# Optimization experiments

Hardware: AMD Instinct MI355X
Metric: run time of the kernel (lower is better)

The kernel has to match this reference:

```python
import jax, jax.numpy as jnp
import numpy as np

N = 2_000_000  # total nodes across batch
F = 16         # eigenvector coefficient dim
B = 8          # number of graphs in batch (2^B sign combos)

def setup_inputs() -> dict:
    key = jax.random.key(0)
    k1, k2, k3 = jax.random.split(key, 3)
    inp = jax.random.normal(k1, (N, F), dtype=jnp.float32)
    tgt = jax.random.normal(k2, (N, F), dtype=jnp.float32)
    batch = jnp.sort(jax.random.randint(k3, (N,), 0, B, dtype=jnp.int32))
    return {"input": inp, "target": tgt, "batch": batch, "batch_size": B}

def reference(input, target, batch, batch_size):
    # loss(s) = sum((s_{batch} * x - t)^2) = sum(x^2) + sum(t^2) - 2 * sum_g s_g * dot_g
    # where dot_g = sum_{i in graph g} <x_i, t_i>.  Min over s in {+1,-1}^B is the
    # exact value produced by the original 2^B brute-force loop (reduction='sum').
    per_node = jnp.sum(input * target, axis=-1)                      # [N]
    dots = jax.ops.segment_sum(per_node, batch, num_segments=batch_size)  # [B]
    base = jnp.sum(input * input) + jnp.sum(target * target)         # scalar
    # enumerate all 2^B sign combinations (tiny, graph-level)
    idx = jnp.arange(2 ** batch_size)
    bits = (idx[:, None] >> jnp.arange(batch_size)[None, :]) & 1     # [2^B, B]
    signs = (1 - 2 * bits).astype(dots.dtype)                        # {+1,-1}
    losses = base - 2.0 * (signs @ dots)                             # [2^B]
    return jnp.min(losses)
```

## Files before the change

kernel.cpp:

```cpp
#include <hip/hip_runtime.h>

#define BLOCK  256
#define NGRAPH 8
#define EBLK   4096
#define NSLOT  8


__global__ __launch_bounds__(BLOCK) void reduce_kernel(
    const float4* __restrict__ x4,
    const float4* __restrict__ t4,
    const int*    __restrict__ batch,
    float* __restrict__ g_acc,
    int M )
{
    __shared__ float s_acc[NGRAPH + 1];
    const int tid = threadIdx.x;
    if (tid < NGRAPH + 1) s_acc[tid] = 0.0f;
    __syncthreads();

    const int elo = (int)blockIdx.x * EBLK;
    const int ehi = min(elo + EBLK, M);

    const int g0 = batch[elo >> 2];
    const int g1 = batch[(ehi - 1) >> 2];

    float base = 0.0f;

    if (g0 == g1) {
        float dot = 0.0f;
        if (ehi == elo + EBLK) {
            #pragma unroll 4
            for (int j = 0; j < EBLK / BLOCK; ++j) {
                const int e = elo + j * BLOCK + tid;
                const float4 a = x4[e];
                const float4 c = t4[e];
                base += a.x*a.x + a.y*a.y + a.z*a.z + a.w*a.w
                      + c.x*c.x + c.y*c.y + c.z*c.z + c.w*c.w;
                dot  += a.x*c.x + a.y*c.y + a.z*c.z + a.w*c.w;
            }
        } else {
            for (int e = elo + tid; e < ehi; e += BLOCK) {
                const float4 a = x4[e];
                const float4 c = t4[e];
                base += a.x*a.x + a.y*a.y + a.z*a.z + a.w*a.w
                      + c.x*c.x + c.y*c.y + c.z*c.z + c.w*c.w;
                dot  += a.x*c.x + a.y*c.y + a.z*c.z + a.w*c.w;
            }
        }
        #pragma unroll
        for (int off = 32; off > 0; off >>= 1) {
            dot  += __shfl_xor(dot,  off, 64);
            base += __shfl_xor(base, off, 64);
        }
        if ((tid & 63) == 0) {
            atomicAdd(&s_acc[g0], dot);
            atomicAdd(&s_acc[NGRAPH], base);
        }
    } else {
        float acc[NGRAPH];
        #pragma unroll
        for (int i = 0; i < NGRAPH; ++i) acc[i] = 0.0f;
        for (int e = elo + tid; e < ehi; e += BLOCK) {
            const float4 a = x4[e];
            const float4 c = t4[e];
            const int    b = batch[e >> 2];
            base += a.x*a.x + a.y*a.y + a.z*a.z + a.w*a.w
                  + c.x*c.x + c.y*c.y + c.z*c.z + c.w*c.w;
            const float d = a.x*c.x + a.y*c.y + a.z*c.z + a.w*c.w;
            #pragma unroll
            for (int i = 0; i < NGRAPH; ++i)
                acc[i] += (b == i) ? d : 0.0f;
        }
        #pragma unroll
        for (int i = 0; i <= NGRAPH; ++i) {
            float v = (i < NGRAPH) ? acc[i] : base;
            #pragma unroll
            for (int off = 32; off > 0; off >>= 1)
                v += __shfl_xor(v, off, 64);
            if ((tid & 63) == 0)
                atomicAdd(&s_acc[i], v);
        }
    }
    __syncthreads();

    float* slot = g_acc + (blockIdx.x & (NSLOT - 1)) * 16;
    if (tid <= NGRAPH)
        atomicAdd(&slot[tid], s_acc[tid]);
}

__global__ void finalize_kernel(const float* __restrict__ g_acc,
                                float* __restrict__ out)
{
    if (threadIdx.x == 0) {
        float dots[NGRAPH];
        #pragma unroll
        for (int i = 0; i < NGRAPH; ++i) dots[i] = 0.0f;
        float base = 0.0f;
        for (int s = 0; s < NSLOT; ++s) {
            #pragma unroll
            for (int i = 0; i < NGRAPH; ++i) dots[i] += g_acc[s * 16 + i];
            base += g_acc[s * 16 + NGRAPH];
        }
        float sum = 0.0f;
        #pragma unroll
        for (int i = 0; i < NGRAPH; ++i) sum += fabsf(dots[i]);
        out[0] = base - 2.0f * sum;
    }
}

extern "C" void kernel_launch(void* const* d_in, const int* in_sizes, int n_in,
                              void* d_out, int out_size, void* d_ws, size_t ws_size,
                              hipStream_t stream) {
    const float* inp   = (const float*)d_in[0];
    const float* tgt   = (const float*)d_in[1];
    const int*   batch = (const int*)d_in[2];

    const long long Nrows = (long long)in_sizes[0] / 16;
    const int       M     = (int)(Nrows * 4);

    float* g_acc = (float*)d_ws;
    hipMemsetAsync(g_acc, 0, NSLOT * 16 * sizeof(float), stream);

    const int nblocks = (M + EBLK - 1) / EBLK;
    reduce_kernel<<<nblocks, BLOCK, 0, stream>>>(
        (const float4*)inp, (const float4*)tgt, batch, g_acc, M);

    finalize_kernel<<<1, 64, 0, stream>>>(g_acc, (float*)d_out);
}
```

Measured before the change: 278.1 us.

## Stage tiles via global_load_lds into LDS and drop shared accumulator

Full single-graph tiles are now loaded straight from global memory into LDS with the direct-to-LDS load builtin, then reduced from LDS with two independent accumulator pairs. The tile size is halved, so the grid has more blocks. The shared-memory accumulator and its two barriers are gone, and each wavefront does its atomic adds directly to the global slot. This spends 64 KB of LDS per block, which limits occupancy, and puts more atomics on the same few global addresses.

```diff
diff --git a/kernel.cpp b/kernel.cpp
--- a/kernel.cpp
+++ b/kernel.cpp
@@ -2,9 +2,12 @@
 
 #define BLOCK  256
 #define NGRAPH 8
-#define EBLK   4096
+#define TE     2048
 #define NSLOT  8
 
+
+#define GPTR(p) ((const __attribute__((address_space(1))) void*)(p))
+#define LPTR(p) ((__attribute__((address_space(3))) void*)(p))
 
 __global__ __launch_bounds__(BLOCK) void reduce_kernel(
     const float4* __restrict__ x4,
@@ -13,53 +16,64 @@
     float* __restrict__ g_acc,
     int M )
 {
-    __shared__ float s_acc[NGRAPH + 1];
-    const int tid = threadIdx.x;
-    if (tid < NGRAPH + 1) s_acc[tid] = 0.0f;
-    __syncthreads();
+    __shared__ float4 sx[TE];
+    __shared__ float4 st[TE];
 
-    const int elo = (int)blockIdx.x * EBLK;
-    const int ehi = min(elo + EBLK, M);
+    const int tid  = threadIdx.x;
+    const int lane = tid & 63;
+    const int w    = tid >> 6;
+
+    const int elo = (int)blockIdx.x * TE;
+    const int ehi = min(elo + TE, M);
 
     const int g0 = batch[elo >> 2];
     const int g1 = batch[(ehi - 1) >> 2];
 
-    float base = 0.0f;
+    float* slot = g_acc + ((int)blockIdx.x & (NSLOT - 1)) * 16;
 
-    if (g0 == g1) {
-        float dot = 0.0f;
-        if (ehi == elo + EBLK) {
-            #pragma unroll 4
-            for (int j = 0; j < EBLK / BLOCK; ++j) {
-                const int e = elo + j * BLOCK + tid;
-                const float4 a = x4[e];
-                const float4 c = t4[e];
-                base += a.x*a.x + a.y*a.y + a.z*a.z + a.w*a.w
-                      + c.x*c.x + c.y*c.y + c.z*c.z + c.w*c.w;
-                dot  += a.x*c.x + a.y*c.y + a.z*c.z + a.w*c.w;
-            }
-        } else {
-            for (int e = elo + tid; e < ehi; e += BLOCK) {
-                const float4 a = x4[e];
-                const float4 c = t4[e];
-                base += a.x*a.x + a.y*a.y + a.z*a.z + a.w*a.w
-                      + c.x*c.x + c.y*c.y + c.z*c.z + c.w*c.w;
-                dot  += a.x*c.x + a.y*c.y + a.z*c.z + a.w*c.w;
-            }
+    if (g0 == g1 && ehi == elo + TE) {
+        const float4* gx = x4 + elo + w * 512 + lane;
+        const float4* gt = t4 + elo + w * 512 + lane;
+        #pragma unroll
+        for (int k = 0; k < 8; ++k)
+            __builtin_amdgcn_global_load_lds(GPTR(gx + k * 64),
+                                             LPTR(&sx[w * 512 + k * 64]), 16, 0, 0);
+        #pragma unroll
+        for (int k = 0; k < 8; ++k)
+            __builtin_amdgcn_global_load_lds(GPTR(gt + k * 64),
+                                             LPTR(&st[w * 512 + k * 64]), 16, 0, 0);
+        __syncthreads();
+
+        float d0 = 0.f, d1 = 0.f, b0 = 0.f, b1 = 0.f;
+        #pragma unroll
+        for (int j = 0; j < 8; j += 2) {
+            const float4 a0 = sx[tid + (j    ) * BLOCK];
+            const float4 c0 = st[tid + (j    ) * BLOCK];
+            const float4 a1 = sx[tid + (j + 1) * BLOCK];
+            const float4 c1 = st[tid + (j + 1) * BLOCK];
+            d0 += a0.x*c0.x + a0.y*c0.y + a0.z*c0.z + a0.w*c0.w;
+            d1 += a1.x*c1.x + a1.y*c1.y + a1.z*c1.z + a1.w*c1.w;
+            b0 += a0.x*a0.x + a0.y*a0.y + a0.z*a0.z + a0.w*a0.w
+                + c0.x*c0.x + c0.y*c0.y + c0.z*c0.z + c0.w*c0.w;
+            b1 += a1.x*a1.x + a1.y*a1.y + a1.z*a1.z + a1.w*a1.w
+                + c1.x*c1.x + c1.y*c1.y + c1.z*c1.z + c1.w*c1.w;
         }
+        float dot = d0 + d1, base = b0 + b1;
+
         #pragma unroll
         for (int off = 32; off > 0; off >>= 1) {
             dot  += __shfl_xor(dot,  off, 64);
             base += __shfl_xor(base, off, 64);
         }
-        if ((tid & 63) == 0) {
-            atomicAdd(&s_acc[g0], dot);
-            atomicAdd(&s_acc[NGRAPH], base);
+        if (lane == 0) {
+            atomicAdd(&slot[g0],     dot);
+            atomicAdd(&slot[NGRAPH], base);
         }
     } else {
         float acc[NGRAPH];
         #pragma unroll
         for (int i = 0; i < NGRAPH; ++i) acc[i] = 0.0f;
+        float base = 0.0f;
         for (int e = elo + tid; e < ehi; e += BLOCK) {
             const float4 a = x4[e];
             const float4 c = t4[e];
@@ -77,15 +91,10 @@
             #pragma unroll
             for (int off = 32; off > 0; off >>= 1)
                 v += __shfl_xor(v, off, 64);
-            if ((tid & 63) == 0)
-                atomicAdd(&s_acc[i], v);
+            if (lane == 0)
+                atomicAdd(&slot[i], v);
         }
     }
-    __syncthreads();
-
-    float* slot = g_acc + (blockIdx.x & (NSLOT - 1)) * 16;
-    if (tid <= NGRAPH)
-        atomicAdd(&slot[tid], s_acc[tid]);
 }
 
 __global__ void finalize_kernel(const float* __restrict__ g_acc,
@@ -121,7 +130,7 @@
     float* g_acc = (float*)d_ws;
     hipMemsetAsync(g_acc, 0, NSLOT * 16 * sizeof(float), stream);
 
-    const int nblocks = (M + EBLK - 1) / EBLK;
+    const int nblocks = (M + TE - 1) / TE;
     reduce_kernel<<<nblocks, BLOCK, 0, stream>>>(
         (const float4*)inp, (const float4*)tgt, batch, g_acc, M);
 
```

Measured after the change: 309.7 us. 11.3% more time.
